# Optimization experiments

Hardware: AMD Instinct MI355X
Metric: run time of the kernel (lower is better)

## Reference

```python
import jax, jax.numpy as jnp
import numpy as np

S, B, H = 512, 64, 1024


def setup_inputs() -> dict:
    key = jax.random.key(0)
    ks = jax.random.split(key, 9)
    sc = 1.0 / np.sqrt(2 * H)
    return {
        "hidden": jax.random.normal(ks[0], (B, H), jnp.float32),
        "decoder_out": jax.random.normal(ks[1], (B, H), jnp.float32),
        "encoder_states": jax.random.normal(ks[2], (S, B, H), jnp.float32),
        "W_attn": jax.random.uniform(ks[3], (2 * H, 2 * H), jnp.float32, -sc, sc),
        "b_attn": jax.random.uniform(ks[4], (2 * H,), jnp.float32, -sc, sc),
        "W_attn2": jax.random.uniform(ks[5], (1, 2 * H), jnp.float32, -sc, sc),
        "b_attn2": jax.random.uniform(ks[6], (1,), jnp.float32, -sc, sc),
        "W_comb": jax.random.uniform(ks[7], (H, 2 * H), jnp.float32, -sc, sc),
        "b_comb": jax.random.uniform(ks[8], (H,), jnp.float32, -sc, sc),
    }


def reference(hidden, decoder_out, encoder_states, W_attn, b_attn, W_attn2, b_attn2, W_comb, b_comb):
    s, b, h = encoder_states.shape
    # per-timestep cat(hidden, enc_t) -> attn -> tanh -> attn2, fully batched over S
    hid = jnp.broadcast_to(hidden[None], (s, b, h))
    cat = jnp.concatenate([hid, encoder_states], axis=-1)            # [S,B,2H]
    scores = jnp.tanh(cat @ W_attn.T + b_attn) @ W_attn2.T + b_attn2  # [S,B,1]
    scores = scores[..., 0].T                                         # [B,S] (stack dim=1 + squeeze)
    attn_w = jax.nn.softmax(scores, axis=-1)                          # [B,S]
    # bmm([B,1,S], [B,S,H]) -> [B,H]
    applied = jnp.einsum("bs,sbh->bh", attn_w, encoder_states)
    out = jnp.concatenate([decoder_out, applied], axis=-1) @ W_comb.T + b_comb
    out = jnp.tanh(out)
    return out, applied
```

## Files before the change

### kernel.cpp

```cpp
#include <hip/hip_runtime.h>
#include <stdint.h>


typedef __attribute__((ext_vector_type(8))) short bf16x8;
typedef __attribute__((ext_vector_type(4))) float f32x4;

__device__ __forceinline__ float bf2f(uint16_t u) {
  return __uint_as_float(((uint32_t)u) << 16);
}
__device__ __forceinline__ uint16_t f2bf(float x) {
  uint32_t u = __float_as_uint(x);
  u += 0x7fffu + ((u >> 16) & 1u);
  return (uint16_t)(u >> 16);
}
__device__ __forceinline__ uint32_t pk2(float a, float b) {
  return (uint32_t)f2bf(a) | ((uint32_t)f2bf(b) << 16);
}
__device__ __forceinline__ uint4 cvt8(const float* __restrict__ p) {
  const float4 a = *(const float4*)p;
  const float4 b = *(const float4*)(p + 4);
  uint4 r;
  r.x = pk2(a.x, a.y); r.y = pk2(a.z, a.w);
  r.z = pk2(b.x, b.y); r.w = pk2(b.z, b.w);
  return r;
}
__device__ __forceinline__ float tanh_fast(float x) {
  const float e = __expf(2.f * x);
  return __builtin_fmaf(-2.f, __builtin_amdgcn_rcpf(e + 1.f), 1.f);
}
__device__ __forceinline__ void load16(const uint16_t* g, uint16_t* l) {
  __builtin_amdgcn_global_load_lds(
      (const __attribute__((address_space(1))) void*)g,
      (__attribute__((address_space(3))) void*)l, 16, 0, 0);
}

__global__ __launch_bounds__(256)
void init_kernel(float* __restrict__ scores, float* __restrict__ U,
                 const float* __restrict__ ba) {
  const int tid = blockIdx.x * 256 + threadIdx.x;
  scores[tid] = 0.f;
#pragma unroll
  for (int k = 0; k < 4; ++k) {
    const int i = tid * 4 + k;
    U[i] = ba[i & 2047];
  }
}

__global__ __launch_bounds__(256)
void cvt_all_kernel(const float* __restrict__ enc, const float* __restrict__ Wa,
                    const float* __restrict__ Wc,
                    uint16_t* __restrict__ enc_bf, uint16_t* __restrict__ Wa_bf,
                    uint16_t* __restrict__ Wc_bf) {
  const int stride = gridDim.x * 256;
  for (int idx = blockIdx.x * 256 + threadIdx.x; idx < 4718592; idx += stride) {
    if (idx < 4194304) {
      ((uint4*)enc_bf)[idx] = cvt8(enc + (size_t)idx * 8);
    } else if (idx < 4456448) {
      const int k = idx - 4194304;
      const int j = k >> 7, c8 = k & 127;
      ((uint4*)Wa_bf)[k] = cvt8(Wa + (size_t)j * 2048 + 1024 + c8 * 8);
    } else {
      const int k = idx - 4456448;
      ((uint4*)Wc_bf)[k] = cvt8(Wc + (size_t)k * 8);
    }
  }
}

__global__ __launch_bounds__(256)
void gemm_u_kernel(const float* __restrict__ A, const float* __restrict__ B32,
                   float* __restrict__ U) {
  __shared__ __align__(16) uint16_t sA[128 * 32];
  __shared__ __align__(16) uint16_t sB[128 * 32];
  const int t = threadIdx.x, lane = t & 63, wave = t >> 6;
  const int wm = wave >> 1, wn = wave & 1;
  const int bn0 = blockIdx.x * 128;
  const int kbase = blockIdx.y * 256;
  const int srow = t >> 2, scol = (t & 3) * 8;
  const int ar0 = min(srow, 63), ar1 = min(64 + srow, 63);
  f32x4 acc[4][4];
#pragma unroll
  for (int i = 0; i < 4; ++i)
#pragma unroll
    for (int j = 0; j < 4; ++j) acc[i][j] = (f32x4){0.f, 0.f, 0.f, 0.f};
  const int mrow = wm * 64 + (lane & 15);
  const int nrow = wn * 64 + (lane & 15);
  const int kq = (lane >> 4) * 8;
  for (int kk = 0; kk < 8; ++kk) {
    const int k0 = kbase + (kk << 5);
    const uint4 va0 = cvt8(A + (size_t)ar0 * 1024 + scol + k0);
    const uint4 va1 = cvt8(A + (size_t)ar1 * 1024 + scol + k0);
    const uint4 vb0 = cvt8(B32 + (size_t)(bn0 + srow) * 2048 + scol + k0);
    const uint4 vb1 = cvt8(B32 + (size_t)(bn0 + 64 + srow) * 2048 + scol + k0);
    __syncthreads();
    *(uint4*)&sA[t * 8] = va0;
    *(uint4*)&sA[2048 + t * 8] = va1;
    *(uint4*)&sB[t * 8] = vb0;
    *(uint4*)&sB[2048 + t * 8] = vb1;
    __syncthreads();
    bf16x8 af[4], bfr[4];
#pragma unroll
    for (int i = 0; i < 4; ++i) af[i] = *(const bf16x8*)&sA[(mrow + i * 16) * 32 + kq];
#pragma unroll
    for (int j = 0; j < 4; ++j) bfr[j] = *(const bf16x8*)&sB[(nrow + j * 16) * 32 + kq];
#pragma unroll
    for (int i = 0; i < 4; ++i)
#pragma unroll
      for (int j = 0; j < 4; ++j)
        acc[i][j] = __builtin_amdgcn_mfma_f32_16x16x32_bf16(af[i], bfr[j], acc[i][j], 0, 0, 0);
  }
  const int colb = lane & 15, rquad = lane >> 4;
#pragma unroll
  for (int i = 0; i < 4; ++i)
#pragma unroll
    for (int r = 0; r < 4; ++r) {
      const int gm = wm * 64 + i * 16 + rquad * 4 + r;
      if (gm < 64) {
#pragma unroll
        for (int j = 0; j < 4; ++j) {
          const int gn = bn0 + wn * 64 + j * 16 + colb;
          atomicAdd(&U[gm * 2048 + gn], acc[i][j][r]);
        }
      }
    }
}

template <int MODE>
__global__ __launch_bounds__(256)
void gemm_bf_kernel(const uint16_t* __restrict__ A, int lda,
                    const uint16_t* __restrict__ Bm, int ldb,
                    int M, int K,
                    float* __restrict__ outf,
                    const float* __restrict__ Ubias,
                    const float* __restrict__ bias) {
  __shared__ __align__(16) uint16_t lds[3][2][4096];

  const int t = threadIdx.x, lane = t & 63, wave = t >> 6;
  const int wm = wave >> 1, wn = wave & 1;
  const int bm0 = blockIdx.x * 128;
  const int bn0 = blockIdx.y * 128;
  const int kbase = (MODE == 3) ? (int)blockIdx.z * 512 : 0;
  const int nt = ((MODE == 3) ? 512 : K) >> 5;

  const uint16_t* gpA[2];
  const uint16_t* gpB[2];
  int sb[2];
#pragma unroll
  for (int q = 0; q < 2; ++q) {
    const int s = q * 256 + t;
    const int r = s >> 2, kc = s & 3;
    const int g = kc ^ ((r >> 1) & 3);
    gpA[q] = A + (size_t)min(bm0 + r, M - 1) * lda + kbase + g * 8;
    gpB[q] = Bm + (size_t)(bn0 + r) * ldb + kbase + g * 8;
    sb[q] = (q * 256 + wave * 64) * 8;
  }

  f32x4 acc[4][4];
#pragma unroll
  for (int i = 0; i < 4; ++i)
#pragma unroll
    for (int j = 0; j < 4; ++j) acc[i][j] = (f32x4){0.f, 0.f, 0.f, 0.f};

  const int swz = ((lane >> 1) & 3) << 3;
  const int kq = ((lane >> 4) * 8) ^ swz;
  const int aoff = (wm * 64 + (lane & 15)) * 32 + kq;
  const int boff = (wn * 64 + (lane & 15)) * 32 + kq;

#pragma unroll
  for (int q = 0; q < 2; ++q) {
    load16(gpA[q], &lds[0][0][sb[q]]);
    load16(gpB[q], &lds[0][1][sb[q]]);
  }
#pragma unroll
  for (int q = 0; q < 2; ++q) {
    load16(gpA[q] + 32, &lds[1][0][sb[q]]);
    load16(gpB[q] + 32, &lds[1][1][sb[q]]);
  }
  asm volatile("s_waitcnt vmcnt(4)" ::: "memory");
  __builtin_amdgcn_s_barrier();

  int cur = 0, nx2 = 2;
  for (int kt = 0; kt < nt; ++kt) {
    const int kpre = (kt + 2 < nt) ? (kt + 2) * 32 : (nt - 1) * 32;
#pragma unroll
    for (int q = 0; q < 2; ++q) {
      load16(gpA[q] + kpre, &lds[nx2][0][sb[q]]);
      load16(gpB[q] + kpre, &lds[nx2][1][sb[q]]);
    }
    const uint16_t* sA = lds[cur][0];
    const uint16_t* sB = lds[cur][1];
    bf16x8 af[4], bfr[4];
#pragma unroll
    for (int i = 0; i < 4; ++i) af[i] = *(const bf16x8*)&sA[aoff + i * 512];
#pragma unroll
    for (int j = 0; j < 4; ++j) bfr[j] = *(const bf16x8*)&sB[boff + j * 512];
#pragma unroll
    for (int i = 0; i < 4; ++i)
#pragma unroll
      for (int j = 0; j < 4; ++j)
        acc[i][j] = __builtin_amdgcn_mfma_f32_16x16x32_bf16(af[i], bfr[j], acc[i][j], 0, 0, 0);
    asm volatile("s_waitcnt vmcnt(4)" ::: "memory");
    __builtin_amdgcn_s_barrier();
    cur = (cur == 2) ? 0 : cur + 1;
    nx2 = (nx2 == 2) ? 0 : nx2 + 1;
  }
  asm volatile("s_waitcnt vmcnt(0)" ::: "memory");

  const int colb = lane & 15, rquad = lane >> 4;
  if (MODE == 1) {
    float w2f[4];
#pragma unroll
    for (int j = 0; j < 4; ++j) w2f[j] = bias[bn0 + wn * 64 + j * 16 + colb];
#pragma unroll
    for (int i = 0; i < 4; ++i) {
#pragma unroll
      for (int r = 0; r < 4; ++r) {
        const int gm = bm0 + wm * 64 + i * 16 + rquad * 4 + r;
        const int bb = gm & 63;
        float p = 0.f;
#pragma unroll
        for (int j = 0; j < 4; ++j) {
          const float u = Ubias[bb * 2048 + bn0 + wn * 64 + j * 16 + colb];
          p += tanh_fast(acc[i][j][r] + u) * w2f[j];
        }
        p += __shfl_xor(p, 1);
        p += __shfl_xor(p, 2);
        p += __shfl_xor(p, 4);
        p += __shfl_xor(p, 8);
        if (colb == 0) atomicAdd(outf + gm, p);
      }
    }
  } else {
    const float bsc = (blockIdx.z == 0) ? 1.f : 0.f;
#pragma unroll
    for (int i = 0; i < 4; ++i)
#pragma unroll
      for (int r = 0; r < 4; ++r) {
        const int gm = bm0 + wm * 64 + i * 16 + rquad * 4 + r;
        if (gm < M) {
#pragma unroll
          for (int j = 0; j < 4; ++j) {
            const int gn = bn0 + wn * 64 + j * 16 + colb;
            atomicAdd(outf + gm * 1024 + gn, acc[i][j][r] + bsc * bias[gn]);
          }
        }
      }
  }
}

__global__ __launch_bounds__(256)
void applied_kernel(const uint16_t* __restrict__ encb, const float* __restrict__ dec,
                    const float* __restrict__ scores,
                    float* __restrict__ out_applied, uint16_t* __restrict__ acat,
                    float* __restrict__ out_acc) {
  const int b = blockIdx.x, chunk = blockIdx.y, t = threadIdx.x;
  const int wave = t >> 6, lane = t & 63;
  __shared__ float w[512];
  __shared__ float red[8];
  __shared__ float2 part2[256];
  float v0 = scores[(size_t)t * 64 + b];
  float v1 = scores[(size_t)(t + 256) * 64 + b];
  float mx = fmaxf(v0, v1);
#pragma unroll
  for (int off = 32; off >= 1; off >>= 1) mx = fmaxf(mx, __shfl_xor(mx, off));
  if (lane == 0) red[wave] = mx;
  __syncthreads();
  mx = fmaxf(fmaxf(red[0], red[1]), fmaxf(red[2], red[3]));
  const float e0 = __expf(v0 - mx), e1 = __expf(v1 - mx);
  float sum = e0 + e1;
#pragma unroll
  for (int off = 32; off >= 1; off >>= 1) sum += __shfl_xor(sum, off);
  if (lane == 0) red[4 + wave] = sum;
  __syncthreads();
  sum = (red[4] + red[5]) + (red[6] + red[7]);
  const float inv = 1.f / sum;
  w[t] = e0 * inv;
  w[t + 256] = e1 * inv;
  __syncthreads();
  const int hp = t & 31, sq = t >> 5;
  const int h = chunk * 64 + hp * 2;
  const uint32_t* base = (const uint32_t*)encb + (size_t)b * 512 + (h >> 1);
  float a0 = 0.f, a1 = 0.f;
#pragma unroll 8
  for (int s = sq * 64; s < sq * 64 + 64; ++s) {
    const uint32_t p = base[(size_t)s * 32768];
    a0 += w[s] * bf2f((uint16_t)(p & 0xffffu));
    a1 += w[s] * bf2f((uint16_t)(p >> 16));
  }
  part2[t] = make_float2(a0, a1);
  __syncthreads();
  if (t < 32) {
    a0 = 0.f; a1 = 0.f;
#pragma unroll
    for (int k = 0; k < 8; ++k) {
      const float2 pp = part2[t + 32 * k];
      a0 += pp.x; a1 += pp.y;
    }
    *(float2*)(out_applied + (size_t)b * 1024 + h) = make_float2(a0, a1);
    *(uint32_t*)(acat + (size_t)b * 2048 + 1024 + h) = pk2(a0, a1);
    *(uint32_t*)(acat + (size_t)b * 2048 + h) =
        pk2(dec[(size_t)b * 1024 + h], dec[(size_t)b * 1024 + h + 1]);
    *(float2*)(out_acc + (size_t)b * 1024 + h) = make_float2(0.f, 0.f);
  }
}

__global__ __launch_bounds__(256)
void tanh_kernel(const float* __restrict__ acc, float* __restrict__ outp) {
  const int i = blockIdx.x * 256 + threadIdx.x;
  float4 v = ((const float4*)acc)[i];
  v.x = tanh_fast(v.x); v.y = tanh_fast(v.y);
  v.z = tanh_fast(v.z); v.w = tanh_fast(v.w);
  ((float4*)outp)[i] = v;
}

extern "C" void kernel_launch(void* const* d_in, const int* in_sizes, int n_in,
                              void* d_out, int out_size, void* d_ws, size_t ws_size,
                              hipStream_t stream) {
  const float* hidden  = (const float*)d_in[0];
  const float* dec     = (const float*)d_in[1];
  const float* enc     = (const float*)d_in[2];
  const float* W_attn  = (const float*)d_in[3];
  const float* b_attn  = (const float*)d_in[4];
  const float* W_attn2 = (const float*)d_in[5];
  const float* W_comb  = (const float*)d_in[7];
  const float* b_comb  = (const float*)d_in[8];
  float* outp = (float*)d_out;

  char* ws = (char*)d_ws;
  float*    scores = (float*)(ws + 0);
  float*    U      = (float*)(ws + 131072);
  float*    out_acc= (float*)(ws + 131072);
  uint16_t* acat   = (uint16_t*)(ws + 655360);
  uint16_t* enc_bf = (uint16_t*)(ws + 1048576);
  uint16_t* Wa_bf  = (uint16_t*)(ws + 68157440);
  uint16_t* Wc_bf  = (uint16_t*)(ws + 72351744);

  init_kernel<<<128, 256, 0, stream>>>(scores, U, b_attn);
  cvt_all_kernel<<<4608, 256, 0, stream>>>(enc, W_attn, W_comb, enc_bf, Wa_bf, Wc_bf);
  gemm_u_kernel<<<dim3(16, 4), 256, 0, stream>>>(hidden, W_attn, U);
  gemm_bf_kernel<1><<<dim3(256, 16), 256, 0, stream>>>(
      enc_bf, 1024, Wa_bf, 1024, 32768, 1024, scores, U, W_attn2);
  applied_kernel<<<dim3(64, 16), 256, 0, stream>>>(enc_bf, dec, scores,
                                                   outp + 65536, acat, out_acc);
  gemm_bf_kernel<3><<<dim3(1, 8, 4), 256, 0, stream>>>(
      acat, 2048, Wc_bf, 2048, 64, 2048, out_acc, nullptr, b_comb);
  tanh_kernel<<<64, 256, 0, stream>>>(out_acc, outp);
}
```

Before: 484.8 us.

## Fold init into convert kernel, XCD-aware tile remap, fully unroll GEMM K loop

Merges the zero/bias init kernel into the bf16 conversion kernel, which removes one launch. The main scoring GEMM now runs on a 1D grid whose block index is remapped so that blocks on the same XCD share A rows, meant to improve L2 reuse of encoder tiles. The GEMM K-loop is made a compile-time constant and fully unrolled, with the redundant tail prefetches and the final barriers dropped. The unrolling raises code size and register pressure, and the remap assumes blocks are dispatched round-robin across the 8 XCDs.

```diff
diff --git a/kernel.cpp b/kernel.cpp
--- a/kernel.cpp
+++ b/kernel.cpp
@@ -35,24 +35,23 @@
 }
 
 __global__ __launch_bounds__(256)
-void init_kernel(float* __restrict__ scores, float* __restrict__ U,
-                 const float* __restrict__ ba) {
-  const int tid = blockIdx.x * 256 + threadIdx.x;
-  scores[tid] = 0.f;
-#pragma unroll
-  for (int k = 0; k < 4; ++k) {
-    const int i = tid * 4 + k;
-    U[i] = ba[i & 2047];
-  }
-}
-
-__global__ __launch_bounds__(256)
 void cvt_all_kernel(const float* __restrict__ enc, const float* __restrict__ Wa,
                     const float* __restrict__ Wc,
                     uint16_t* __restrict__ enc_bf, uint16_t* __restrict__ Wa_bf,
-                    uint16_t* __restrict__ Wc_bf) {
+                    uint16_t* __restrict__ Wc_bf,
+                    float* __restrict__ scores, float* __restrict__ U,
+                    const float* __restrict__ ba) {
+  const int tid0 = blockIdx.x * 256 + threadIdx.x;
+  if (tid0 < 32768) {
+    scores[tid0] = 0.f;
+#pragma unroll
+    for (int k = 0; k < 4; ++k) {
+      const int i = tid0 * 4 + k;
+      U[i] = ba[i & 2047];
+    }
+  }
   const int stride = gridDim.x * 256;
-  for (int idx = blockIdx.x * 256 + threadIdx.x; idx < 4718592; idx += stride) {
+  for (int idx = tid0; idx < 4718592; idx += stride) {
     if (idx < 4194304) {
       ((uint4*)enc_bf)[idx] = cvt8(enc + (size_t)idx * 8);
     } else if (idx < 4456448) {
@@ -124,22 +123,29 @@
     }
 }
 
-template <int MODE>
+template <int MODE, int NT>
 __global__ __launch_bounds__(256)
 void gemm_bf_kernel(const uint16_t* __restrict__ A, int lda,
                     const uint16_t* __restrict__ Bm, int ldb,
-                    int M, int K,
-                    float* __restrict__ outf,
+                    int M, float* __restrict__ outf,
                     const float* __restrict__ Ubias,
                     const float* __restrict__ bias) {
   __shared__ __align__(16) uint16_t lds[3][2][4096];
 
   const int t = threadIdx.x, lane = t & 63, wave = t >> 6;
   const int wm = wave >> 1, wn = wave & 1;
-  const int bm0 = blockIdx.x * 128;
-  const int bn0 = blockIdx.y * 128;
-  const int kbase = (MODE == 3) ? (int)blockIdx.z * 512 : 0;
-  const int nt = ((MODE == 3) ? 512 : K) >> 5;
+  int bm0, bn0, kbase;
+  if (MODE == 1) {
+    const int wid = blockIdx.x;
+    const int xcd = wid & 7, q = wid >> 3;
+    bm0 = (xcd * 32 + (q >> 4)) * 128;
+    bn0 = (q & 15) * 128;
+    kbase = 0;
+  } else {
+    bm0 = 0;
+    bn0 = blockIdx.y * 128;
+    kbase = blockIdx.z * (NT * 32);
+  }
 
   const uint16_t* gpA[2];
   const uint16_t* gpB[2];
@@ -178,16 +184,20 @@
   asm volatile("s_waitcnt vmcnt(4)" ::: "memory");
   __builtin_amdgcn_s_barrier();
 
-  int cur = 0, nx2 = 2;
-  for (int kt = 0; kt < nt; ++kt) {
-    const int kpre = (kt + 2 < nt) ? (kt + 2) * 32 : (nt - 1) * 32;
-#pragma unroll
-    for (int q = 0; q < 2; ++q) {
-      load16(gpA[q] + kpre, &lds[nx2][0][sb[q]]);
-      load16(gpB[q] + kpre, &lds[nx2][1][sb[q]]);
-    }
-    const uint16_t* sA = lds[cur][0];
-    const uint16_t* sB = lds[cur][1];
+#pragma unroll
+  for (int kt = 0; kt < NT; ++kt) {
+    const int bufc = kt % 3;
+    if (kt + 2 < NT) {
+      const int nb = (kt + 2) % 3;
+      const int kpre = (kt + 2) * 32;
+#pragma unroll
+      for (int q = 0; q < 2; ++q) {
+        load16(gpA[q] + kpre, &lds[nb][0][sb[q]]);
+        load16(gpB[q] + kpre, &lds[nb][1][sb[q]]);
+      }
+    }
+    const uint16_t* sA = lds[bufc][0];
+    const uint16_t* sB = lds[bufc][1];
     bf16x8 af[4], bfr[4];
 #pragma unroll
     for (int i = 0; i < 4; ++i) af[i] = *(const bf16x8*)&sA[aoff + i * 512];
@@ -198,12 +208,14 @@
 #pragma unroll
       for (int j = 0; j < 4; ++j)
         acc[i][j] = __builtin_amdgcn_mfma_f32_16x16x32_bf16(af[i], bfr[j], acc[i][j], 0, 0, 0);
-    asm volatile("s_waitcnt vmcnt(4)" ::: "memory");
-    __builtin_amdgcn_s_barrier();
-    cur = (cur == 2) ? 0 : cur + 1;
-    nx2 = (nx2 == 2) ? 0 : nx2 + 1;
-  }
-  asm volatile("s_waitcnt vmcnt(0)" ::: "memory");
+    if (kt + 2 < NT) {
+      asm volatile("s_waitcnt vmcnt(4) lgkmcnt(0)" ::: "memory");
+      __builtin_amdgcn_s_barrier();
+    } else if (kt + 1 < NT) {
+      asm volatile("s_waitcnt vmcnt(0) lgkmcnt(0)" ::: "memory");
+      __builtin_amdgcn_s_barrier();
+    }
+  }
 
   const int colb = lane & 15, rquad = lane >> 4;
   if (MODE == 1) {
@@ -334,14 +346,14 @@
   uint16_t* Wa_bf  = (uint16_t*)(ws + 68157440);
   uint16_t* Wc_bf  = (uint16_t*)(ws + 72351744);
 
-  init_kernel<<<128, 256, 0, stream>>>(scores, U, b_attn);
-  cvt_all_kernel<<<4608, 256, 0, stream>>>(enc, W_attn, W_comb, enc_bf, Wa_bf, Wc_bf);
+  cvt_all_kernel<<<4608, 256, 0, stream>>>(enc, W_attn, W_comb, enc_bf, Wa_bf,
+                                           Wc_bf, scores, U, b_attn);
   gemm_u_kernel<<<dim3(16, 4), 256, 0, stream>>>(hidden, W_attn, U);
-  gemm_bf_kernel<1><<<dim3(256, 16), 256, 0, stream>>>(
-      enc_bf, 1024, Wa_bf, 1024, 32768, 1024, scores, U, W_attn2);
+  gemm_bf_kernel<1, 32><<<4096, 256, 0, stream>>>(
+      enc_bf, 1024, Wa_bf, 1024, 32768, scores, U, W_attn2);
   applied_kernel<<<dim3(64, 16), 256, 0, stream>>>(enc_bf, dec, scores,
                                                    outp + 65536, acat, out_acc);
-  gemm_bf_kernel<3><<<dim3(1, 8, 4), 256, 0, stream>>>(
-      acat, 2048, Wc_bf, 2048, 64, 2048, out_acc, nullptr, b_comb);
+  gemm_bf_kernel<3, 16><<<dim3(1, 8, 4), 256, 0, stream>>>(
+      acat, 2048, Wc_bf, 2048, 64, out_acc, nullptr, b_comb);
   tanh_kernel<<<64, 256, 0, stream>>>(out_acc, outp);
 }
```

After: 456.9 us. 1.06x faster.
